# Kernel tuning notes

Measured on AMD Instinct MI355X. Metric: run time of the kernel, lower is better.

## Reference

```python
import jax, jax.numpy as jnp
import numpy as np

B, S, D = 2, 2048, 1024
M = 2048          # d_mlp
E = 8             # num_experts
TOP_K = 2


def setup_inputs() -> dict:
    key = jax.random.key(0)
    ks = jax.random.split(key, 5)
    std = 0.02
    return {
        "residual": jax.random.normal(ks[0], (B, S, D), jnp.float32),
        "W_router": jax.random.normal(ks[1], (D, E), jnp.float32) * std,
        "W_gate": jax.random.normal(ks[2], (E, D, M), jnp.float32) * std,
        "b_gate": jnp.zeros((E, M), jnp.float32),
        "W_up": jax.random.normal(ks[3], (E, D, M), jnp.float32) * std,
        "b_up": jnp.zeros((E, M), jnp.float32),
        "W_out": jax.random.normal(ks[4], (E, M, D), jnp.float32) * std,
        "b_out": jnp.zeros((E, D), jnp.float32),
    }


def reference(residual, W_router, W_gate, b_gate, W_up, b_up, W_out, b_out):
    # --- router: softmax over experts, top-k selection, renormalize ---
    router_logits = jnp.einsum('bsd,de->bse', residual, W_router)
    router_probs = jax.nn.softmax(router_logits, axis=-1)
    top_k_probs, top_k_idx = jax.lax.top_k(router_probs, TOP_K)          # [B,S,K]
    top_k_probs = top_k_probs / (jnp.sum(top_k_probs, -1, keepdims=True) + 1e-8)
    # per-expert combine weight [B,S,E]; top-k indices are unique per token
    one_hot = jax.nn.one_hot(top_k_idx, E, dtype=residual.dtype)          # [B,S,K,E]
    expert_weights = jnp.einsum('bsk,bske->bse', top_k_probs, one_hot)
    # --- each expert runs dense SwiGLU MLP on the FULL batch (compute-then-mask, as in source) ---
    gate = jax.nn.silu(jnp.einsum('bsd,edm->ebsm', residual, W_gate) + b_gate[:, None, None, :])
    up = jnp.einsum('bsd,edm->ebsm', residual, W_up) + b_up[:, None, None, :]
    hidden = gate * up                                                    # [E,B,S,M]
    expert_out = jnp.einsum('ebsm,emd->ebsd', hidden, W_out) + b_out[:, None, None, :]
    # --- weighted combine (weights are zero for non-selected experts) ---
    output = jnp.einsum('bse,ebsd->bsd', expert_weights, expert_out)
    return output
```

## Files before the change

### kernel.cpp

```cpp
#include <hip/hip_runtime.h>
#include <cstdint>
#include <cstddef>

#define TT 4096
#define DD 1024
#define MM 2048
#define EE 8
#define NPAIR 8192

typedef unsigned short u16;
typedef __bf16 bf16x8 __attribute__((ext_vector_type(8)));
typedef float f32x4 __attribute__((ext_vector_type(4)));
typedef u16 u16x8 __attribute__((ext_vector_type(8)));
typedef __attribute__((address_space(3))) void* lds_vp;
typedef __attribute__((address_space(1))) const void* gbl_cvp;

__device__ __forceinline__ void async16(u16* l, const u16* g) {
  __builtin_amdgcn_global_load_lds((gbl_cvp)(const void*)g, (lds_vp)(void*)l, 16, 0, 0);
}

__device__ __forceinline__ u16 f2bf(float f) {
  uint32_t u = __builtin_bit_cast(uint32_t, f);
  u += 0x7fffu + ((u >> 16) & 1u);
  return (u16)(u >> 16);
}
__device__ __forceinline__ float bf2f(u16 h) {
  uint32_t u = ((uint32_t)h) << 16;
  return __builtin_bit_cast(float, u);
}

__global__ void router_kernel(const float* __restrict__ X, const float* __restrict__ Wr,
                              int* __restrict__ tok_idx, float* __restrict__ wpair,
                              u16* __restrict__ Xbf) {
  int wave = threadIdx.x >> 6;
  int lane = threadIdx.x & 63;
  int t = blockIdx.x * 4 + wave;
  const float4* x4 = (const float4*)(X + (size_t)t * DD);
  float acc[EE];
#pragma unroll
  for (int e = 0; e < EE; e++) acc[e] = 0.f;
#pragma unroll
  for (int i = 0; i < 4; i++) {
    float4 xv = x4[i * 64 + lane];
    ushort4 o;
    o.x = f2bf(xv.x); o.y = f2bf(xv.y); o.z = f2bf(xv.z); o.w = f2bf(xv.w);
    *(ushort4*)&Xbf[(size_t)t * DD + (size_t)(i * 64 + lane) * 4] = o;
    const float4* wr4 = (const float4*)(Wr + (size_t)(i * 256 + lane * 4) * EE);
    float xs[4] = {xv.x, xv.y, xv.z, xv.w};
#pragma unroll
    for (int c = 0; c < 4; c++) {
      float4 wa = wr4[c * 2 + 0];
      float4 wb = wr4[c * 2 + 1];
      acc[0] += xs[c] * wa.x; acc[1] += xs[c] * wa.y;
      acc[2] += xs[c] * wa.z; acc[3] += xs[c] * wa.w;
      acc[4] += xs[c] * wb.x; acc[5] += xs[c] * wb.y;
      acc[6] += xs[c] * wb.z; acc[7] += xs[c] * wb.w;
    }
  }
#pragma unroll
  for (int off = 32; off > 0; off >>= 1)
#pragma unroll
    for (int e = 0; e < EE; e++) acc[e] += __shfl_xor(acc[e], off);
  if (lane == 0) {
    float mx = acc[0];
#pragma unroll
    for (int e = 1; e < EE; e++) mx = fmaxf(mx, acc[e]);
    float p[EE], s = 0.f;
#pragma unroll
    for (int e = 0; e < EE; e++) { p[e] = __expf(acc[e] - mx); s += p[e]; }
    float inv = 1.f / s;
#pragma unroll
    for (int e = 0; e < EE; e++) p[e] *= inv;
    int i0 = 0;
#pragma unroll
    for (int e = 1; e < EE; e++) if (p[e] > p[i0]) i0 = e;
    int i1 = (i0 == 0) ? 1 : 0;
#pragma unroll
    for (int e = 0; e < EE; e++) if (e != i0 && p[e] > p[i1]) i1 = e;
    float denom = p[i0] + p[i1] + 1e-8f;
    tok_idx[t * 2 + 0] = i0;
    tok_idx[t * 2 + 1] = i1;
    wpair[t * 2 + 0] = p[i0] / denom;
    wpair[t * 2 + 1] = p[i1] / denom;
  }
}

__global__ void bucket_kernel(const int* __restrict__ tok_idx, int* __restrict__ offsets,
                              int* __restrict__ bucket) {
  __shared__ int lcnt[EE];
  __shared__ int lcur[EE];
  int tid = threadIdx.x;
  if (tid < EE) lcnt[tid] = 0;
  __syncthreads();
  for (int i = tid; i < NPAIR; i += 1024) atomicAdd(&lcnt[tok_idx[i]], 1);
  __syncthreads();
  if (tid == 0) {
    int s = 0;
    for (int e = 0; e < EE; e++) {
      offsets[e] = s;
      lcur[e] = s;
      s += lcnt[e];
    }
    offsets[EE] = s;
  }
  __syncthreads();
  for (int i = tid; i < NPAIR; i += 1024) {
    int e = tok_idx[i];
    int pos = atomicAdd(&lcur[e], 1);
    bucket[pos] = i;
  }
}

__global__ __launch_bounds__(256)
void transpose_cvt(const float* __restrict__ in, u16* __restrict__ out, int R, int C) {
  __shared__ float tile[64][65];
  int e = blockIdx.z;
  const float* I = in + (size_t)e * R * C;
  u16* O = out + (size_t)e * R * C;
  int c0 = blockIdx.x * 64, r0 = blockIdx.y * 64;
  int t = threadIdx.x;
  {
    int cq = t & 15;
    int rb = t >> 4;
#pragma unroll
    for (int i = 0; i < 4; i++) {
      int r = rb + i * 16;
      float4 v = *(const float4*)&I[(size_t)(r0 + r) * C + c0 + cq * 4];
      tile[cq * 4 + 0][r] = v.x;
      tile[cq * 4 + 1][r] = v.y;
      tile[cq * 4 + 2][r] = v.z;
      tile[cq * 4 + 3][r] = v.w;
    }
  }
  __syncthreads();
  {
    int rseg = (t & 7) * 8;
    int cc = t >> 3;
#pragma unroll
    for (int i = 0; i < 2; i++) {
      int c = cc + i * 32;
      u16x8 o;
#pragma unroll
      for (int k = 0; k < 8; k++) o[k] = f2bf(tile[c][rseg + k]);
      *(u16x8*)&O[(size_t)(c0 + c) * R + r0 + rseg] = o;
    }
  }
}

__device__ __forceinline__ bool tile_map(const int* __restrict__ offsets, int x,
                                         int& expert, int& row0, int& rows) {
  expert = -1;
#pragma unroll 1
  for (int e = 0; e < EE; e++) {
    int o0 = offsets[e], o1 = offsets[e + 1];
    int nt = (o1 - o0 + 127) >> 7;
    if (x < nt) { expert = e; row0 = o0 + (x << 7); rows = min(128, o1 - row0); return true; }
    x -= nt;
  }
  return false;
}

template <int NTLOG2>
__device__ __forceinline__ void grid_decode(int bid, int& rt, int& n0) {
  int xcd = bid & 7, slot = bid >> 3;
  rt = xcd * 9 + (slot >> NTLOG2);
  n0 = (slot & ((1 << NTLOG2) - 1)) * 128;
}


template <int MODE>
__global__ __launch_bounds__(256)
void moe_gemm(const u16* __restrict__ Aglob, const u16* __restrict__ Wt,
              const float* __restrict__ bias, u16* __restrict__ Hws,
              float* __restrict__ Ypart, const int* __restrict__ offsets,
              const int* __restrict__ bucket, const float* __restrict__ wpair) {
  constexpr int K = (MODE == 2) ? MM : DD;
  constexpr int N = (MODE == 2) ? DD : MM;

  int rt, n0;
  grid_decode<(MODE == 2) ? 3 : 4>(blockIdx.x, rt, n0);
  int expert, row0, rows;
  if (!tile_map(offsets, rt, expert, row0, rows)) return;

  __shared__ u16 Alds[128 * 32];
  __shared__ u16 Blds[128 * 32];

  int tid = threadIdx.x;
  int wave = tid >> 6, lane = tid & 63;
  int wm = wave >> 1, wn = wave & 1;
  int quad = lane >> 4, l15 = lane & 15;
  int swz = ((lane & 3) ^ ((lane >> 3) & 3)) * 8;
  int rp  = (quad ^ ((l15 >> 1) & 3)) * 8;

  long arow0, arow1;
  {
    int r0l = wave * 32 + (lane >> 2);
    int rr0 = min(r0l, rows - 1);
    int rr1 = min(r0l + 16, rows - 1);
    if (MODE == 2) {
      arow0 = (long)(row0 + rr0) * K;
      arow1 = (long)(row0 + rr1) * K;
    } else {
      arow0 = (long)(bucket[row0 + rr0] >> 1) * K;
      arow1 = (long)(bucket[row0 + rr1] >> 1) * K;
    }
  }
  const u16* A0 = Aglob + arow0 + swz;
  const u16* A1 = Aglob + arow1 + swz;
  const u16* B0 = Wt + (size_t)expert * N * K + (size_t)n0 * K
                  + (long)(wave * 32 + (lane >> 2)) * K + swz;
  const u16* B1 = B0 + 16 * K;

  u16* sA0 = &Alds[(wave * 32) * 32]; u16* sA1 = &Alds[(wave * 32 + 16) * 32];
  u16* sB0 = &Blds[(wave * 32) * 32]; u16* sB1 = &Blds[(wave * 32 + 16) * 32];

  f32x4 acc[4][4];
#pragma unroll
  for (int i = 0; i < 4; i++)
#pragma unroll
    for (int j = 0; j < 4; j++) acc[i][j] = (f32x4){0, 0, 0, 0};

  for (int k0 = 0; k0 < K; k0 += 32) {
    async16(sA0, A0); async16(sA1, A1);
    async16(sB0, B0); async16(sB1, B1);
    A0 += 32; A1 += 32; B0 += 32; B1 += 32;
    __syncthreads();
    bf16x8 af[4], bf[4];
#pragma unroll
    for (int i = 0; i < 4; i++) {
      af[i] = *(const bf16x8*)&Alds[(wm * 64 + i * 16 + l15) * 32 + rp];
      bf[i] = *(const bf16x8*)&Blds[(wn * 64 + i * 16 + l15) * 32 + rp];
    }
#pragma unroll
    for (int i = 0; i < 4; i++)
#pragma unroll
      for (int j = 0; j < 4; j++)
        acc[i][j] = __builtin_amdgcn_mfma_f32_16x16x32_bf16(af[i], bf[j], acc[i][j], 0, 0, 0);
    __syncthreads();
  }

#pragma unroll
  for (int i = 0; i < 4; i++) {
    int lrb = wm * 64 + i * 16 + quad * 4;
#pragma unroll
    for (int j = 0; j < 4; j++) {
      int gc = n0 + wn * 64 + j * 16 + l15;
      float bv = bias[expert * N + gc];
#pragma unroll
      for (int r = 0; r < 4; r++) {
        int lr = lrb + r;
        if (lr < rows) {
          int grow = row0 + lr;
          float v = acc[i][j][r] + bv;
          if (MODE == 0) {
            Hws[(size_t)grow * MM + gc] = f2bf(v);
          } else if (MODE == 1) {
            float u = bf2f(Hws[(size_t)grow * MM + gc]);
            float sg = v / (1.f + __expf(-v));
            Hws[(size_t)grow * MM + gc] = f2bf(sg * u);
          } else {
            int p = bucket[grow];
            float w = wpair[p];
            Ypart[(size_t)p * DD + gc] = w * v;
          }
        }
      }
    }
  }
}

__global__ void combine_kernel(const float* __restrict__ Ypart, float* __restrict__ out) {
  int i = blockIdx.x * 256 + threadIdx.x;
  int t = i >> 8;
  int c4 = i & 255;
  const float4* y0 = (const float4*)(Ypart + (size_t)(2 * t) * DD) + c4;
  const float4* y1 = (const float4*)(Ypart + (size_t)(2 * t + 1) * DD) + c4;
  float4 a = *y0, b = *y1;
  float4 o;
  o.x = a.x + b.x; o.y = a.y + b.y; o.z = a.z + b.z; o.w = a.w + b.w;
  ((float4*)out)[i] = o;
}

extern "C" void kernel_launch(void* const* d_in, const int* in_sizes, int n_in,
                              void* d_out, int out_size, void* d_ws, size_t ws_size,
                              hipStream_t stream) {
  const float* residual = (const float*)d_in[0];
  const float* W_router = (const float*)d_in[1];
  const float* W_gate   = (const float*)d_in[2];
  const float* b_gate   = (const float*)d_in[3];
  const float* W_up     = (const float*)d_in[4];
  const float* b_up     = (const float*)d_in[5];
  const float* W_out    = (const float*)d_in[6];
  const float* b_out    = (const float*)d_in[7];
  float* out = (float*)d_out;

  char* ws = (char*)d_ws;
  int*   tok_idx = (int*)(ws + 0);
  float* wpair   = (float*)(ws + 32768);
  int*   offsets = (int*)(ws + 65536);
  int*   bucket  = (int*)(ws + 65536 + 512);
  u16*   Xbf  = (u16*)(ws + 131072);
  u16*   WtG  = Xbf + (size_t)TT * DD;
  u16*   WtU  = WtG + (size_t)EE * MM * DD;
  u16*   WtO  = WtU + (size_t)EE * MM * DD;
  u16*   Hws  = WtO + (size_t)EE * DD * MM;
  float* Ypart = (float*)(Hws + (size_t)NPAIR * MM);

  router_kernel<<<dim3(TT / 4), dim3(256), 0, stream>>>(residual, W_router, tok_idx, wpair, Xbf);
  bucket_kernel<<<dim3(1), dim3(1024), 0, stream>>>(tok_idx, offsets, bucket);
  transpose_cvt<<<dim3(MM / 64, DD / 64, EE), dim3(256), 0, stream>>>(W_gate, WtG, DD, MM);
  transpose_cvt<<<dim3(MM / 64, DD / 64, EE), dim3(256), 0, stream>>>(W_up,   WtU, DD, MM);
  transpose_cvt<<<dim3(DD / 64, MM / 64, EE), dim3(256), 0, stream>>>(W_out,  WtO, MM, DD);
  moe_gemm<0><<<dim3(8 * 9 * 16), dim3(256), 0, stream>>>(Xbf, WtU, b_up,   Hws, Ypart, offsets, bucket, wpair);
  moe_gemm<1><<<dim3(8 * 9 * 16), dim3(256), 0, stream>>>(Xbf, WtG, b_gate, Hws, Ypart, offsets, bucket, wpair);
  moe_gemm<2><<<dim3(8 * 9 * 8),  dim3(256), 0, stream>>>(Hws, WtO, b_out,  Hws, Ypart, offsets, bucket, wpair);
  combine_kernel<<<dim3(TT * DD / 4 / 256), dim3(256), 0, stream>>>(Ypart, out);
}
```

Before: 478.6 us.

## Fuse gate and up GEMMs into one kernel and double-buffer LDS tiles

Replaces the separate up-projection and gate-projection launches with one kernel that loads each activation tile once, accumulates both the gate and up products, and applies SiLU·up in the epilogue. This removes the bf16 round-trip of the up result through the hidden workspace and one full pass over the gathered activations. Both GEMM kernels also gain double-buffered LDS staging, so the async loads for the next K-slice overlap the MFMA work on the current one. The cost is twice the accumulator registers in the fused kernel, capped by a launch bound of two blocks per CU, which may cause spills or lower occupancy.

```diff
diff --git a/kernel.cpp b/kernel.cpp
--- a/kernel.cpp
+++ b/kernel.cpp
@@ -168,22 +168,19 @@
 }
 
 
-template <int MODE>
-__global__ __launch_bounds__(256)
-void moe_gemm(const u16* __restrict__ Aglob, const u16* __restrict__ Wt,
-              const float* __restrict__ bias, u16* __restrict__ Hws,
-              float* __restrict__ Ypart, const int* __restrict__ offsets,
-              const int* __restrict__ bucket, const float* __restrict__ wpair) {
-  constexpr int K = (MODE == 2) ? MM : DD;
-  constexpr int N = (MODE == 2) ? DD : MM;
-
+__global__ __launch_bounds__(256, 2)
+void moe_gemm_gu(const u16* __restrict__ Xbf, const u16* __restrict__ WtG,
+                 const u16* __restrict__ WtU, const float* __restrict__ bgate,
+                 const float* __restrict__ bup, u16* __restrict__ Hws,
+                 const int* __restrict__ offsets, const int* __restrict__ bucket) {
   int rt, n0;
-  grid_decode<(MODE == 2) ? 3 : 4>(blockIdx.x, rt, n0);
+  grid_decode<4>(blockIdx.x, rt, n0);
   int expert, row0, rows;
   if (!tile_map(offsets, rt, expert, row0, rows)) return;
 
-  __shared__ u16 Alds[128 * 32];
-  __shared__ u16 Blds[128 * 32];
+  __shared__ u16 Alds[2][128 * 32];
+  __shared__ u16 Glds[2][128 * 32];
+  __shared__ u16 Ulds[2][128 * 32];
 
   int tid = threadIdx.x;
   int wave = tid >> 6, lane = tid & 63;
@@ -197,45 +194,58 @@
     int r0l = wave * 32 + (lane >> 2);
     int rr0 = min(r0l, rows - 1);
     int rr1 = min(r0l + 16, rows - 1);
-    if (MODE == 2) {
-      arow0 = (long)(row0 + rr0) * K;
-      arow1 = (long)(row0 + rr1) * K;
-    } else {
-      arow0 = (long)(bucket[row0 + rr0] >> 1) * K;
-      arow1 = (long)(bucket[row0 + rr1] >> 1) * K;
-    }
-  }
-  const u16* A0 = Aglob + arow0 + swz;
-  const u16* A1 = Aglob + arow1 + swz;
-  const u16* B0 = Wt + (size_t)expert * N * K + (size_t)n0 * K
-                  + (long)(wave * 32 + (lane >> 2)) * K + swz;
-  const u16* B1 = B0 + 16 * K;
-
-  u16* sA0 = &Alds[(wave * 32) * 32]; u16* sA1 = &Alds[(wave * 32 + 16) * 32];
-  u16* sB0 = &Blds[(wave * 32) * 32]; u16* sB1 = &Blds[(wave * 32 + 16) * 32];
-
-  f32x4 acc[4][4];
+    arow0 = (long)(bucket[row0 + rr0] >> 1) * DD;
+    arow1 = (long)(bucket[row0 + rr1] >> 1) * DD;
+  }
+  const u16* A0 = Xbf + arow0 + swz;
+  const u16* A1 = Xbf + arow1 + swz;
+  size_t bo = (size_t)expert * MM * DD + (size_t)n0 * DD
+            + (long)(wave * 32 + (lane >> 2)) * DD + swz;
+  const u16* G0 = WtG + bo; const u16* G1 = G0 + 16 * DD;
+  const u16* U0 = WtU + bo; const u16* U1 = U0 + 16 * DD;
+
+  int sb0 = (wave * 32) * 32, sb1 = (wave * 32 + 16) * 32;
+
+  f32x4 accG[4][4], accU[4][4];
 #pragma unroll
   for (int i = 0; i < 4; i++)
 #pragma unroll
-    for (int j = 0; j < 4; j++) acc[i][j] = (f32x4){0, 0, 0, 0};
-
-  for (int k0 = 0; k0 < K; k0 += 32) {
-    async16(sA0, A0); async16(sA1, A1);
-    async16(sB0, B0); async16(sB1, B1);
-    A0 += 32; A1 += 32; B0 += 32; B1 += 32;
-    __syncthreads();
+    for (int j = 0; j < 4; j++) { accG[i][j] = (f32x4){0,0,0,0}; accU[i][j] = (f32x4){0,0,0,0}; }
+
+  auto stage = [&](int b) {
+    async16(&Alds[b][sb0], A0); async16(&Alds[b][sb1], A1);
+    async16(&Glds[b][sb0], G0); async16(&Glds[b][sb1], G1);
+    async16(&Ulds[b][sb0], U0); async16(&Ulds[b][sb1], U1);
+    A0 += 32; A1 += 32; G0 += 32; G1 += 32; U0 += 32; U1 += 32;
+  };
+
+  stage(0);
+  __syncthreads();
+
+  constexpr int NT = DD / 32;
+#pragma unroll 2
+  for (int t = 0; t < NT; ++t) {
+    int cur = t & 1;
+    if (t + 1 < NT) stage(cur ^ 1);
     bf16x8 af[4], bf[4];
 #pragma unroll
     for (int i = 0; i < 4; i++) {
-      af[i] = *(const bf16x8*)&Alds[(wm * 64 + i * 16 + l15) * 32 + rp];
-      bf[i] = *(const bf16x8*)&Blds[(wn * 64 + i * 16 + l15) * 32 + rp];
+      af[i] = *(const bf16x8*)&Alds[cur][(wm * 64 + i * 16 + l15) * 32 + rp];
+      bf[i] = *(const bf16x8*)&Glds[cur][(wn * 64 + i * 16 + l15) * 32 + rp];
     }
 #pragma unroll
     for (int i = 0; i < 4; i++)
 #pragma unroll
       for (int j = 0; j < 4; j++)
-        acc[i][j] = __builtin_amdgcn_mfma_f32_16x16x32_bf16(af[i], bf[j], acc[i][j], 0, 0, 0);
+        accG[i][j] = __builtin_amdgcn_mfma_f32_16x16x32_bf16(af[i], bf[j], accG[i][j], 0, 0, 0);
+#pragma unroll
+    for (int i = 0; i < 4; i++)
+      bf[i] = *(const bf16x8*)&Ulds[cur][(wn * 64 + i * 16 + l15) * 32 + rp];
+#pragma unroll
+    for (int i = 0; i < 4; i++)
+#pragma unroll
+      for (int j = 0; j < 4; j++)
+        accU[i][j] = __builtin_amdgcn_mfma_f32_16x16x32_bf16(af[i], bf[j], accU[i][j], 0, 0, 0);
     __syncthreads();
   }
 
@@ -245,24 +255,108 @@
 #pragma unroll
     for (int j = 0; j < 4; j++) {
       int gc = n0 + wn * 64 + j * 16 + l15;
-      float bv = bias[expert * N + gc];
+      float bg = bgate[expert * MM + gc];
+      float bu = bup[expert * MM + gc];
 #pragma unroll
       for (int r = 0; r < 4; r++) {
         int lr = lrb + r;
         if (lr < rows) {
           int grow = row0 + lr;
-          float v = acc[i][j][r] + bv;
-          if (MODE == 0) {
-            Hws[(size_t)grow * MM + gc] = f2bf(v);
-          } else if (MODE == 1) {
-            float u = bf2f(Hws[(size_t)grow * MM + gc]);
-            float sg = v / (1.f + __expf(-v));
-            Hws[(size_t)grow * MM + gc] = f2bf(sg * u);
-          } else {
-            int p = bucket[grow];
-            float w = wpair[p];
-            Ypart[(size_t)p * DD + gc] = w * v;
-          }
+          float g = accG[i][j][r] + bg;
+          float u = accU[i][j][r] + bu;
+          float sg = g / (1.f + __expf(-g));
+          Hws[(size_t)grow * MM + gc] = f2bf(sg * u);
+        }
+      }
+    }
+  }
+}
+
+__global__ __launch_bounds__(256)
+void moe_gemm_out(const u16* __restrict__ Hmat, const u16* __restrict__ WtO,
+                  const float* __restrict__ bias, float* __restrict__ Ypart,
+                  const int* __restrict__ offsets, const int* __restrict__ bucket,
+                  const float* __restrict__ wpair) {
+  int rt, n0;
+  grid_decode<3>(blockIdx.x, rt, n0);
+  int expert, row0, rows;
+  if (!tile_map(offsets, rt, expert, row0, rows)) return;
+
+  __shared__ u16 Alds[2][128 * 32];
+  __shared__ u16 Blds[2][128 * 32];
+
+  int tid = threadIdx.x;
+  int wave = tid >> 6, lane = tid & 63;
+  int wm = wave >> 1, wn = wave & 1;
+  int quad = lane >> 4, l15 = lane & 15;
+  int swz = ((lane & 3) ^ ((lane >> 3) & 3)) * 8;
+  int rp  = (quad ^ ((l15 >> 1) & 3)) * 8;
+
+  long arow0, arow1;
+  {
+    int r0l = wave * 32 + (lane >> 2);
+    int rr0 = min(r0l, rows - 1);
+    int rr1 = min(r0l + 16, rows - 1);
+    arow0 = (long)(row0 + rr0) * MM;
+    arow1 = (long)(row0 + rr1) * MM;
+  }
+  const u16* A0 = Hmat + arow0 + swz;
+  const u16* A1 = Hmat + arow1 + swz;
+  const u16* B0 = WtO + (size_t)expert * DD * MM + (size_t)n0 * MM
+                + (long)(wave * 32 + (lane >> 2)) * MM + swz;
+  const u16* B1 = B0 + 16 * MM;
+
+  int sb0 = (wave * 32) * 32, sb1 = (wave * 32 + 16) * 32;
+
+  f32x4 acc[4][4];
+#pragma unroll
+  for (int i = 0; i < 4; i++)
+#pragma unroll
+    for (int j = 0; j < 4; j++) acc[i][j] = (f32x4){0, 0, 0, 0};
+
+  auto stage = [&](int b) {
+    async16(&Alds[b][sb0], A0); async16(&Alds[b][sb1], A1);
+    async16(&Blds[b][sb0], B0); async16(&Blds[b][sb1], B1);
+    A0 += 32; A1 += 32; B0 += 32; B1 += 32;
+  };
+
+  stage(0);
+  __syncthreads();
+
+  constexpr int NT = MM / 32;
+#pragma unroll 2
+  for (int t = 0; t < NT; ++t) {
+    int cur = t & 1;
+    if (t + 1 < NT) stage(cur ^ 1);
+    bf16x8 af[4], bf[4];
+#pragma unroll
+    for (int i = 0; i < 4; i++) {
+      af[i] = *(const bf16x8*)&Alds[cur][(wm * 64 + i * 16 + l15) * 32 + rp];
+      bf[i] = *(const bf16x8*)&Blds[cur][(wn * 64 + i * 16 + l15) * 32 + rp];
+    }
+#pragma unroll
+    for (int i = 0; i < 4; i++)
+#pragma unroll
+      for (int j = 0; j < 4; j++)
+        acc[i][j] = __builtin_amdgcn_mfma_f32_16x16x32_bf16(af[i], bf[j], acc[i][j], 0, 0, 0);
+    __syncthreads();
+  }
+
+#pragma unroll
+  for (int i = 0; i < 4; i++) {
+    int lrb = wm * 64 + i * 16 + quad * 4;
+#pragma unroll
+    for (int j = 0; j < 4; j++) {
+      int gc = n0 + wn * 64 + j * 16 + l15;
+      float bv = bias[expert * DD + gc];
+#pragma unroll
+      for (int r = 0; r < 4; r++) {
+        int lr = lrb + r;
+        if (lr < rows) {
+          int grow = row0 + lr;
+          int p = bucket[grow];
+          float w = wpair[p];
+          Ypart[(size_t)p * DD + gc] = w * (acc[i][j][r] + bv);
         }
       }
     }
@@ -311,8 +405,7 @@
   transpose_cvt<<<dim3(MM / 64, DD / 64, EE), dim3(256), 0, stream>>>(W_gate, WtG, DD, MM);
   transpose_cvt<<<dim3(MM / 64, DD / 64, EE), dim3(256), 0, stream>>>(W_up,   WtU, DD, MM);
   transpose_cvt<<<dim3(DD / 64, MM / 64, EE), dim3(256), 0, stream>>>(W_out,  WtO, MM, DD);
-  moe_gemm<0><<<dim3(8 * 9 * 16), dim3(256), 0, stream>>>(Xbf, WtU, b_up,   Hws, Ypart, offsets, bucket, wpair);
-  moe_gemm<1><<<dim3(8 * 9 * 16), dim3(256), 0, stream>>>(Xbf, WtG, b_gate, Hws, Ypart, offsets, bucket, wpair);
-  moe_gemm<2><<<dim3(8 * 9 * 8),  dim3(256), 0, stream>>>(Hws, WtO, b_out,  Hws, Ypart, offsets, bucket, wpair);
+  moe_gemm_gu<<<dim3(8 * 9 * 16), dim3(256), 0, stream>>>(Xbf, WtG, WtU, b_gate, b_up, Hws, offsets, bucket);
+  moe_gemm_out<<<dim3(8 * 9 * 8), dim3(256), 0, stream>>>(Hws, WtO, b_out, Ypart, offsets, bucket, wpair);
   combine_kernel<<<dim3(TT * DD / 4 / 256), dim3(256), 0, stream>>>(Ypart, out);
 }
```

Measured after the change: 467.8 us. 2.2% less time.
